# Kernel optimization log

Hardware: AMD Instinct MI355X
Metric: run time of the kernel (lower is better)

The kernel has to match this reference:

```python
import jax, jax.numpy as jnp
import numpy as np

D_MODEL = 1024
NUM_HEADS = 16
HEAD_DIM = D_MODEL // NUM_HEADS


def setup_inputs() -> dict:
    key = jax.random.key(0)
    k1, k2, k3, k4, k5 = jax.random.split(key, 5)
    B, S = 2, 2048
    X = jax.random.normal(k1, (B, S, D_MODEL), dtype=jnp.float32)
    Wqkv = jax.random.normal(k2, (3 * D_MODEL, D_MODEL), dtype=jnp.float32) * 0.02
    bqkv = jax.random.normal(k3, (3 * D_MODEL,), dtype=jnp.float32) * 0.02
    Wo = jax.random.normal(k4, (D_MODEL, D_MODEL), dtype=jnp.float32) * 0.02
    bo = jax.random.normal(k5, (D_MODEL,), dtype=jnp.float32) * 0.02
    return {"X": X, "Wqkv": Wqkv, "bqkv": bqkv, "Wo": Wo, "bo": bo}


def reference(X, Wqkv, bqkv, Wo, bo):
    B, S, D = X.shape
    # fused QKV projection (torch Linear: x @ W.T + b)
    qkv = X @ Wqkv.T + bqkv                                  # [B, S, 3D]
    qkv = qkv.reshape(B, S, NUM_HEADS, 3 * HEAD_DIM)
    qkv = jnp.transpose(qkv, (0, 2, 1, 3))                   # [B, H, S, 3*hd]
    q, k, v = jnp.split(qkv, 3, axis=-1)                     # each [B, H, S, hd]
    # naive scaled dot-product attention (materializes full SxS scores)
    scale = 1.0 / jnp.sqrt(jnp.asarray(HEAD_DIM, dtype=X.dtype))
    scores = jnp.einsum("bhqd,bhkd->bhqk", q, k) * scale     # [B, H, S, S]
    attn = jax.nn.softmax(scores, axis=-1)
    values = jnp.einsum("bhqk,bhkd->bhqd", attn, v)          # [B, H, S, hd]
    values = jnp.transpose(values, (0, 2, 1, 3)).reshape(B, S, D)
    return values @ Wo.T + bo
```

## Files before the change

kernel.cpp:

```cpp
#include <hip/hip_runtime.h>

#define DM    1024
#define NH    16
#define HD    64
#define SEQ   2048
#define BATCH 2
#define NQKV  3072
#define MTOT  4096

using half4 = __attribute__((ext_vector_type(4))) _Float16;
using half8 = __attribute__((ext_vector_type(8))) _Float16;
using f32x4 = __attribute__((ext_vector_type(4))) float;

typedef const __attribute__((address_space(1))) unsigned int* gp_t;
typedef __attribute__((address_space(3))) unsigned int* lp_t;

__device__ __forceinline__ void gl2lds16(const void* g, void* l) {
    __builtin_amdgcn_global_load_lds((gp_t)g, (lp_t)l, 16, 0, 0);
}

__device__ __forceinline__ f32x4 fzero4() {
    f32x4 v; v[0] = 0.f; v[1] = 0.f; v[2] = 0.f; v[3] = 0.f; return v;
}

__device__ __forceinline__ int sw8(int row, int col) {
    return (row << 6) | ((((col >> 3) ^ row) & 7) << 3) | (col & 7);
}
__device__ __forceinline__ int sw16(int row, int col) {
    return (row << 7) | ((((col >> 3) ^ row) & 15) << 3) | (col & 7);
}

__global__ __launch_bounds__(256) void cvt_f32_f16(const float* __restrict__ in,
                                                   _Float16* __restrict__ out, int n4) {
    int i = blockIdx.x * 256 + threadIdx.x;
    if (i >= n4) return;
    float4 f = reinterpret_cast<const float4*>(in)[i];
    half4 h;
    h[0] = (_Float16)f.x; h[1] = (_Float16)f.y;
    h[2] = (_Float16)f.z; h[3] = (_Float16)f.w;
    reinterpret_cast<half4*>(out)[i] = h;
}

template <bool OUT_F16>
__global__ __launch_bounds__(256) void gemm_nt(const _Float16* __restrict__ A,
                                               const _Float16* __restrict__ B,
                                               const float* __restrict__ bias,
                                               void* __restrict__ Cout,
                                               int M, int N, int K) {
    __shared__ _Float16 lA[128 * 64];
    __shared__ _Float16 lB[128 * 64];
    const int tid = threadIdx.x;
    const int m0 = blockIdx.y * 128, n0 = blockIdx.x * 128;
    const int wave = tid >> 6, lane = tid & 63, quad = lane >> 4, l15 = lane & 15;
    const int wm = (wave & 1) * 64, wn = (wave >> 1) * 64;

    f32x4 acc[4][4];
#pragma unroll
    for (int i = 0; i < 4; ++i)
#pragma unroll
        for (int j = 0; j < 4; ++j) acc[i][j] = fzero4();

    const int cperm = (((tid & 7) ^ (tid >> 3)) & 7) * 8;
    const _Float16* Ab = A + (long)(m0 + (tid >> 3)) * K + cperm;
    const _Float16* Bb = B + (long)(n0 + (tid >> 3)) * K + cperm;
    char* lAp = (char*)lA + tid * 16;
    char* lBp = (char*)lB + tid * 16;

    for (int kt = 0; kt < K; kt += 64) {
        __syncthreads();
#pragma unroll
        for (int j = 0; j < 4; ++j) {
            gl2lds16(Ab + (long)j * 32 * K + kt, lAp + j * 4096);
            gl2lds16(Bb + (long)j * 32 * K + kt, lBp + j * 4096);
        }
        __syncthreads();
#pragma unroll
        for (int ks = 0; ks < 2; ++ks) {
            half8 af[4], bfr[4];
#pragma unroll
            for (int t = 0; t < 4; ++t) {
                af[t]  = *(const half8*)(lA + sw8(wm + t * 16 + l15, ks * 32 + quad * 8));
                bfr[t] = *(const half8*)(lB + sw8(wn + t * 16 + l15, ks * 32 + quad * 8));
            }
#pragma unroll
            for (int mt = 0; mt < 4; ++mt)
#pragma unroll
                for (int nt = 0; nt < 4; ++nt)
                    acc[mt][nt] = __builtin_amdgcn_mfma_f32_16x16x32_f16(
                        af[mt], bfr[nt], acc[mt][nt], 0, 0, 0);
        }
    }

    float bs[4];
#pragma unroll
    for (int nt = 0; nt < 4; ++nt) bs[nt] = bias[n0 + wn + nt * 16 + l15];

#pragma unroll
    for (int mt = 0; mt < 4; ++mt) {
#pragma unroll
        for (int r = 0; r < 4; ++r) {
            const int m = m0 + wm + mt * 16 + quad * 4 + r;
#pragma unroll
            for (int nt = 0; nt < 4; ++nt) {
                const int n = n0 + wn + nt * 16 + l15;
                const float v = acc[mt][nt][r] + bs[nt];
                if constexpr (OUT_F16)
                    ((_Float16*)Cout)[(long)m * N + n] = (_Float16)v;
                else
                    ((float*)Cout)[(long)m * N + n] = v;
            }
        }
    }
}

__global__ __launch_bounds__(256) void repack_v(const _Float16* __restrict__ qkvh,
                                                _Float16* __restrict__ vt) {
    const int b = blockIdx.z, h = blockIdx.y, s0 = blockIdx.x * 32;
    const int d = threadIdx.x & 63, si = threadIdx.x >> 6;
    const _Float16* src = qkvh + (long)(b * SEQ + s0 + si * 8) * NQKV + h * 192 + 128 + d;
    half8 v;
#pragma unroll
    for (int i = 0; i < 8; ++i) v[i] = src[(long)i * NQKV];
    *(half8*)(vt + (long)((b * NH + h) * HD + d) * SEQ + s0 + si * 8) = v;
}

__global__ __launch_bounds__(256) void attn_flash(const _Float16* __restrict__ qkv,
                                                  const _Float16* __restrict__ vt,
                                                  _Float16* __restrict__ aout) {
    __shared__ _Float16 lQ[128 * 64];
    __shared__ _Float16 lK[128 * 64];
    __shared__ _Float16 lV[64 * 128];
    const int b = blockIdx.z, h = blockIdx.y, q0 = blockIdx.x * 128;
    const int tid = threadIdx.x;
    const int wave = tid >> 6, lane = tid & 63, quad = lane >> 4, l15 = lane & 15;
    const float CS = 0.18033688011112042f;

    const int cperm8  = (((tid & 7) ^ (tid >> 3)) & 7) * 8;
    const int cperm16 = (((tid & 15) ^ (tid >> 4)) & 15) * 8;

    const _Float16* qsrc = qkv + (long)(b * SEQ + q0 + (tid >> 3)) * NQKV + h * 192 + cperm8;
#pragma unroll
    for (int j = 0; j < 4; ++j)
        gl2lds16(qsrc + (long)j * 32 * NQKV, (char*)lQ + j * 4096 + tid * 16);
    __syncthreads();

    half8 qf[2][2];
#pragma unroll
    for (int qt = 0; qt < 2; ++qt)
#pragma unroll
        for (int ks = 0; ks < 2; ++ks)
            qf[qt][ks] = *(const half8*)(lQ + sw8(wave * 32 + qt * 16 + l15, ks * 32 + quad * 8));

    f32x4 O[2][4];
#pragma unroll
    for (int qt = 0; qt < 2; ++qt)
#pragma unroll
        for (int dt = 0; dt < 4; ++dt) O[qt][dt] = fzero4();
    float mst[2] = {-1e30f, -1e30f};
    float lst[2] = {0.f, 0.f};

    const _Float16* ksrc = qkv + (long)(b * SEQ + (tid >> 3)) * NQKV + h * 192 + 64 + cperm8;
    const _Float16* vsrc = vt + (long)((b * NH + h) * HD + (tid >> 4)) * SEQ + cperm16;

    for (int it = 0; it < 16; ++it) {
        const int s0 = it * 128;
        __syncthreads();
#pragma unroll
        for (int j = 0; j < 4; ++j) {
            gl2lds16(ksrc + (long)(s0 + j * 32) * NQKV, (char*)lK + j * 4096 + tid * 16);
            gl2lds16(vsrc + (long)j * 16 * SEQ + s0,    (char*)lV + j * 4096 + tid * 16);
        }
        __syncthreads();

        f32x4 st[2][8];
#pragma unroll
        for (int qt = 0; qt < 2; ++qt)
#pragma unroll
            for (int kt = 0; kt < 8; ++kt) st[qt][kt] = fzero4();
#pragma unroll
        for (int kt = 0; kt < 8; ++kt) {
#pragma unroll
            for (int ks = 0; ks < 2; ++ks) {
                half8 kf = *(const half8*)(lK + sw8(kt * 16 + l15, ks * 32 + quad * 8));
                st[0][kt] = __builtin_amdgcn_mfma_f32_16x16x32_f16(kf, qf[0][ks], st[0][kt], 0, 0, 0);
                st[1][kt] = __builtin_amdgcn_mfma_f32_16x16x32_f16(kf, qf[1][ks], st[1][kt], 0, 0, 0);
            }
        }

        float alpha[2];
#pragma unroll
        for (int qt = 0; qt < 2; ++qt) {
            float mc = -1e30f;
#pragma unroll
            for (int kt = 0; kt < 8; ++kt) {
                f32x4 s = st[qt][kt];
                mc = fmaxf(mc, fmaxf(fmaxf(s[0], s[1]), fmaxf(s[2], s[3])));
            }
            mc = fmaxf(mc, __shfl_xor(mc, 16));
            mc = fmaxf(mc, __shfl_xor(mc, 32));
            mc *= CS;
            const float mn = fmaxf(mst[qt], mc);
            alpha[qt] = __builtin_amdgcn_exp2f(mst[qt] - mn);
            mst[qt] = mn;
            float rs = 0.f;
#pragma unroll
            for (int kt = 0; kt < 8; ++kt) {
#pragma unroll
                for (int r = 0; r < 4; ++r) {
                    const float p = __builtin_amdgcn_exp2f(st[qt][kt][r] * CS - mn);
                    st[qt][kt][r] = p;
                    rs += p;
                }
            }
            rs += __shfl_xor(rs, 16);
            rs += __shfl_xor(rs, 32);
            lst[qt] = lst[qt] * alpha[qt] + rs;
        }

#pragma unroll
        for (int qt = 0; qt < 2; ++qt) {
#pragma unroll
            for (int r = 0; r < 4; ++r) {
                const float ar = __shfl(alpha[qt], quad * 4 + r);
#pragma unroll
                for (int dt = 0; dt < 4; ++dt) O[qt][dt][r] *= ar;
            }
        }

#pragma unroll
        for (int t = 0; t < 4; ++t) {
            half8 pf0, pf1;
#pragma unroll
            for (int r = 0; r < 4; ++r) {
                pf0[r]     = (_Float16)st[0][2 * t][r];
                pf0[4 + r] = (_Float16)st[0][2 * t + 1][r];
                pf1[r]     = (_Float16)st[1][2 * t][r];
                pf1[4 + r] = (_Float16)st[1][2 * t + 1][r];
            }
#pragma unroll
            for (int dt = 0; dt < 4; ++dt) {
                const int vrow = dt * 16 + l15;
                half4 v0 = *(const half4*)(lV + sw16(vrow, t * 32 + quad * 4));
                half4 v1 = *(const half4*)(lV + sw16(vrow, t * 32 + quad * 4 + 16));
                half8 vf = __builtin_shufflevector(v0, v1, 0, 1, 2, 3, 4, 5, 6, 7);
                O[0][dt] = __builtin_amdgcn_mfma_f32_16x16x32_f16(pf0, vf, O[0][dt], 0, 0, 0);
                O[1][dt] = __builtin_amdgcn_mfma_f32_16x16x32_f16(pf1, vf, O[1][dt], 0, 0, 0);
            }
        }
    }

#pragma unroll
    for (int qt = 0; qt < 2; ++qt) {
        const float linv = 1.0f / lst[qt];
#pragma unroll
        for (int r = 0; r < 4; ++r) {
            const float lr = __shfl(linv, quad * 4 + r);
            const int row = b * SEQ + q0 + wave * 32 + qt * 16 + quad * 4 + r;
#pragma unroll
            for (int dt = 0; dt < 4; ++dt)
                aout[(long)row * DM + h * HD + dt * 16 + l15] =
                    (_Float16)(O[qt][dt][r] * lr);
        }
    }
}

extern "C" void kernel_launch(void* const* d_in, const int* in_sizes, int n_in,
                              void* d_out, int out_size, void* d_ws, size_t ws_size,
                              hipStream_t stream) {
    const float* X    = (const float*)d_in[0];
    const float* Wqkv = (const float*)d_in[1];
    const float* bqkv = (const float*)d_in[2];
    const float* Wo   = (const float*)d_in[3];
    const float* bo   = (const float*)d_in[4];

    char* ws = (char*)d_ws;
    _Float16* Xh   = (_Float16*)(ws);
    _Float16* Wqh  = (_Float16*)(ws + (size_t)8  * 1048576);
    _Float16* Woh  = (_Float16*)(ws + (size_t)14 * 1048576);
    _Float16* qkvh = (_Float16*)(ws + (size_t)16 * 1048576);
    _Float16* vth  = (_Float16*)(ws + (size_t)40 * 1048576);
    _Float16* atth = (_Float16*)(ws + (size_t)48 * 1048576);

    cvt_f32_f16<<<(MTOT * DM / 4 + 255) / 256, 256, 0, stream>>>(X, Xh, MTOT * DM / 4);
    cvt_f32_f16<<<(NQKV * DM / 4 + 255) / 256, 256, 0, stream>>>(Wqkv, Wqh, NQKV * DM / 4);
    cvt_f32_f16<<<(DM * DM / 4 + 255) / 256, 256, 0, stream>>>(Wo, Woh, DM * DM / 4);

    gemm_nt<true><<<dim3(NQKV / 128, MTOT / 128), 256, 0, stream>>>(
        Xh, Wqh, bqkv, qkvh, MTOT, NQKV, DM);

    repack_v<<<dim3(SEQ / 32, NH, BATCH), 256, 0, stream>>>(qkvh, vth);

    attn_flash<<<dim3(SEQ / 128, NH, BATCH), 256, 0, stream>>>(qkvh, vth, atth);

    gemm_nt<false><<<dim3(DM / 128, MTOT / 128), 256, 0, stream>>>(
        atth, Woh, bo, d_out, MTOT, DM, DM);
}
```

Baseline: 207.3 us.

## Double-buffer attention K/V, compute row sums via MFMA, merge conversions, smaller output GEMM tile

The attention kernel now double-buffers its K/V tiles in shared memory. It prefetches the next block while computing on the current one, and reuses the K buffer to stage Q. Exponentials are computed with fused FMA and packed straight to fp16. Row sums come from an MFMA against a ones vector instead of scalar adds and shuffles, which also drops the final reciprocal shuffle. The three fp32-to-fp16 conversion launches are merged into one kernel writing a contiguous workspace, and the output projection uses a 64-row tile GEMM to double its block count. Together these aim to cut load stalls, VALU work in the softmax, launch overhead and under-filled output GEMM waves, at the cost of doubled attention LDS and slightly different rounding of the denominator.

```diff
diff --git a/kernel.cpp b/kernel.cpp
--- a/kernel.cpp
+++ b/kernel.cpp
@@ -8,9 +8,10 @@
 #define NQKV  3072
 #define MTOT  4096
 
-using half4 = __attribute__((ext_vector_type(4))) _Float16;
-using half8 = __attribute__((ext_vector_type(8))) _Float16;
-using f32x4 = __attribute__((ext_vector_type(4))) float;
+using half2v = __attribute__((ext_vector_type(2))) _Float16;
+using half4  = __attribute__((ext_vector_type(4))) _Float16;
+using half8  = __attribute__((ext_vector_type(8))) _Float16;
+using f32x4  = __attribute__((ext_vector_type(4))) float;
 
 typedef const __attribute__((address_space(1))) unsigned int* gp_t;
 typedef __attribute__((address_space(3))) unsigned int* lp_t;
@@ -30,11 +31,27 @@
     return (row << 7) | ((((col >> 3) ^ row) & 15) << 3) | (col & 7);
 }
 
-__global__ __launch_bounds__(256) void cvt_f32_f16(const float* __restrict__ in,
-                                                   _Float16* __restrict__ out, int n4) {
+#define CSCALE 0.18033688011112042f
+
+__device__ __forceinline__ half2v expk2(float a, float b, float negmn) {
+    return __builtin_bit_cast(half2v, __builtin_amdgcn_cvt_pkrtz(
+        __builtin_amdgcn_exp2f(__builtin_fmaf(a, CSCALE, negmn)),
+        __builtin_amdgcn_exp2f(__builtin_fmaf(b, CSCALE, negmn))));
+}
+
+__global__ __launch_bounds__(256) void cvt_all(const float* __restrict__ X,
+                                               const float* __restrict__ W1,
+                                               const float* __restrict__ W2,
+                                               _Float16* __restrict__ out) {
+    const int nX = MTOT * DM / 4, nW1 = NQKV * DM / 4, nW2 = DM * DM / 4;
     int i = blockIdx.x * 256 + threadIdx.x;
-    if (i >= n4) return;
-    float4 f = reinterpret_cast<const float4*>(in)[i];
+    if (i >= nX + nW1 + nW2) return;
+    const float* src;
+    int off;
+    if (i < nX)            { src = X;  off = i; }
+    else if (i < nX + nW1) { src = W1; off = i - nX; }
+    else                   { src = W2; off = i - nX - nW1; }
+    float4 f = reinterpret_cast<const float4*>(src)[off];
     half4 h;
     h[0] = (_Float16)f.x; h[1] = (_Float16)f.y;
     h[2] = (_Float16)f.z; h[3] = (_Float16)f.w;
@@ -113,6 +130,80 @@
     }
 }
 
+template <bool OUT_F16>
+__global__ __launch_bounds__(256) void gemm_nt_64(const _Float16* __restrict__ A,
+                                                  const _Float16* __restrict__ B,
+                                                  const float* __restrict__ bias,
+                                                  void* __restrict__ Cout,
+                                                  int M, int N, int K) {
+    __shared__ _Float16 lA[64 * 64];
+    __shared__ _Float16 lB[128 * 64];
+    const int tid = threadIdx.x;
+    const int m0 = blockIdx.y * 64, n0 = blockIdx.x * 128;
+    const int wave = tid >> 6, lane = tid & 63, quad = lane >> 4, l15 = lane & 15;
+    const int wm = (wave & 1) * 32, wn = (wave >> 1) * 64;
+
+    f32x4 acc[2][4];
+#pragma unroll
+    for (int i = 0; i < 2; ++i)
+#pragma unroll
+        for (int j = 0; j < 4; ++j) acc[i][j] = fzero4();
+
+    const int cperm = (((tid & 7) ^ (tid >> 3)) & 7) * 8;
+    const _Float16* Ab = A + (long)(m0 + (tid >> 3)) * K + cperm;
+    const _Float16* Bb = B + (long)(n0 + (tid >> 3)) * K + cperm;
+    char* lAp = (char*)lA + tid * 16;
+    char* lBp = (char*)lB + tid * 16;
+
+    for (int kt = 0; kt < K; kt += 64) {
+        __syncthreads();
+#pragma unroll
+        for (int j = 0; j < 2; ++j)
+            gl2lds16(Ab + (long)j * 32 * K + kt, lAp + j * 4096);
+#pragma unroll
+        for (int j = 0; j < 4; ++j)
+            gl2lds16(Bb + (long)j * 32 * K + kt, lBp + j * 4096);
+        __syncthreads();
+#pragma unroll
+        for (int ks = 0; ks < 2; ++ks) {
+            half8 af[2], bfr[4];
+#pragma unroll
+            for (int t = 0; t < 2; ++t)
+                af[t] = *(const half8*)(lA + sw8(wm + t * 16 + l15, ks * 32 + quad * 8));
+#pragma unroll
+            for (int t = 0; t < 4; ++t)
+                bfr[t] = *(const half8*)(lB + sw8(wn + t * 16 + l15, ks * 32 + quad * 8));
+#pragma unroll
+            for (int mt = 0; mt < 2; ++mt)
+#pragma unroll
+                for (int nt = 0; nt < 4; ++nt)
+                    acc[mt][nt] = __builtin_amdgcn_mfma_f32_16x16x32_f16(
+                        af[mt], bfr[nt], acc[mt][nt], 0, 0, 0);
+        }
+    }
+
+    float bs[4];
+#pragma unroll
+    for (int nt = 0; nt < 4; ++nt) bs[nt] = bias[n0 + wn + nt * 16 + l15];
+
+#pragma unroll
+    for (int mt = 0; mt < 2; ++mt) {
+#pragma unroll
+        for (int r = 0; r < 4; ++r) {
+            const int m = m0 + wm + mt * 16 + quad * 4 + r;
+#pragma unroll
+            for (int nt = 0; nt < 4; ++nt) {
+                const int n = n0 + wn + nt * 16 + l15;
+                const float v = acc[mt][nt][r] + bs[nt];
+                if constexpr (OUT_F16)
+                    ((_Float16*)Cout)[(long)m * N + n] = (_Float16)v;
+                else
+                    ((float*)Cout)[(long)m * N + n] = v;
+            }
+        }
+    }
+}
+
 __global__ __launch_bounds__(256) void repack_v(const _Float16* __restrict__ qkvh,
                                                 _Float16* __restrict__ vt) {
     const int b = blockIdx.z, h = blockIdx.y, s0 = blockIdx.x * 32;
@@ -127,13 +218,11 @@
 __global__ __launch_bounds__(256) void attn_flash(const _Float16* __restrict__ qkv,
                                                   const _Float16* __restrict__ vt,
                                                   _Float16* __restrict__ aout) {
-    __shared__ _Float16 lQ[128 * 64];
-    __shared__ _Float16 lK[128 * 64];
-    __shared__ _Float16 lV[64 * 128];
+    __shared__ _Float16 lK[2][128 * 64];
+    __shared__ _Float16 lV[2][64 * 128];
     const int b = blockIdx.z, h = blockIdx.y, q0 = blockIdx.x * 128;
     const int tid = threadIdx.x;
     const int wave = tid >> 6, lane = tid & 63, quad = lane >> 4, l15 = lane & 15;
-    const float CS = 0.18033688011112042f;
 
     const int cperm8  = (((tid & 7) ^ (tid >> 3)) & 7) * 8;
     const int cperm16 = (((tid & 15) ^ (tid >> 4)) & 15) * 8;
@@ -141,7 +230,7 @@
     const _Float16* qsrc = qkv + (long)(b * SEQ + q0 + (tid >> 3)) * NQKV + h * 192 + cperm8;
 #pragma unroll
     for (int j = 0; j < 4; ++j)
-        gl2lds16(qsrc + (long)j * 32 * NQKV, (char*)lQ + j * 4096 + tid * 16);
+        gl2lds16(qsrc + (long)j * 32 * NQKV, (char*)lK[0] + j * 4096 + tid * 16);
     __syncthreads();
 
     half8 qf[2][2];
@@ -149,28 +238,41 @@
     for (int qt = 0; qt < 2; ++qt)
 #pragma unroll
         for (int ks = 0; ks < 2; ++ks)
-            qf[qt][ks] = *(const half8*)(lQ + sw8(wave * 32 + qt * 16 + l15, ks * 32 + quad * 8));
+            qf[qt][ks] = *(const half8*)(lK[0] + sw8(wave * 32 + qt * 16 + l15, ks * 32 + quad * 8));
+    __syncthreads();
 
     f32x4 O[2][4];
 #pragma unroll
     for (int qt = 0; qt < 2; ++qt)
 #pragma unroll
         for (int dt = 0; dt < 4; ++dt) O[qt][dt] = fzero4();
+    f32x4 lsum[2] = {fzero4(), fzero4()};
     float mst[2] = {-1e30f, -1e30f};
-    float lst[2] = {0.f, 0.f};
+
+    half8 ones;
+#pragma unroll
+    for (int i = 0; i < 8; ++i) ones[i] = (_Float16)1.0f;
 
     const _Float16* ksrc = qkv + (long)(b * SEQ + (tid >> 3)) * NQKV + h * 192 + 64 + cperm8;
     const _Float16* vsrc = vt + (long)((b * NH + h) * HD + (tid >> 4)) * SEQ + cperm16;
 
+#pragma unroll
+    for (int j = 0; j < 4; ++j) {
+        gl2lds16(ksrc + (long)(j * 32) * NQKV, (char*)lK[0] + j * 4096 + tid * 16);
+        gl2lds16(vsrc + (long)j * 16 * SEQ,    (char*)lV[0] + j * 4096 + tid * 16);
+    }
+
+    int cur = 0;
     for (int it = 0; it < 16; ++it) {
-        const int s0 = it * 128;
-        __syncthreads();
-#pragma unroll
-        for (int j = 0; j < 4; ++j) {
-            gl2lds16(ksrc + (long)(s0 + j * 32) * NQKV, (char*)lK + j * 4096 + tid * 16);
-            gl2lds16(vsrc + (long)j * 16 * SEQ + s0,    (char*)lV + j * 4096 + tid * 16);
-        }
-        __syncthreads();
+        __syncthreads();
+        if (it < 15) {
+            const int s0n = (it + 1) * 128;
+#pragma unroll
+            for (int j = 0; j < 4; ++j) {
+                gl2lds16(ksrc + (long)(s0n + j * 32) * NQKV, (char*)lK[cur ^ 1] + j * 4096 + tid * 16);
+                gl2lds16(vsrc + (long)j * 16 * SEQ + s0n,    (char*)lV[cur ^ 1] + j * 4096 + tid * 16);
+            }
+        }
 
         f32x4 st[2][8];
 #pragma unroll
@@ -181,13 +283,13 @@
         for (int kt = 0; kt < 8; ++kt) {
 #pragma unroll
             for (int ks = 0; ks < 2; ++ks) {
-                half8 kf = *(const half8*)(lK + sw8(kt * 16 + l15, ks * 32 + quad * 8));
+                half8 kf = *(const half8*)(lK[cur] + sw8(kt * 16 + l15, ks * 32 + quad * 8));
                 st[0][kt] = __builtin_amdgcn_mfma_f32_16x16x32_f16(kf, qf[0][ks], st[0][kt], 0, 0, 0);
                 st[1][kt] = __builtin_amdgcn_mfma_f32_16x16x32_f16(kf, qf[1][ks], st[1][kt], 0, 0, 0);
             }
         }
 
-        float alpha[2];
+        float alpha[2], negmn[2];
 #pragma unroll
         for (int qt = 0; qt < 2; ++qt) {
             float mc = -1e30f;
@@ -198,23 +300,11 @@
             }
             mc = fmaxf(mc, __shfl_xor(mc, 16));
             mc = fmaxf(mc, __shfl_xor(mc, 32));
-            mc *= CS;
+            mc *= CSCALE;
             const float mn = fmaxf(mst[qt], mc);
             alpha[qt] = __builtin_amdgcn_exp2f(mst[qt] - mn);
             mst[qt] = mn;
-            float rs = 0.f;
-#pragma unroll
-            for (int kt = 0; kt < 8; ++kt) {
-#pragma unroll
-                for (int r = 0; r < 4; ++r) {
-                    const float p = __builtin_amdgcn_exp2f(st[qt][kt][r] * CS - mn);
-                    st[qt][kt][r] = p;
-                    rs += p;
-                }
-            }
-            rs += __shfl_xor(rs, 16);
-            rs += __shfl_xor(rs, 32);
-            lst[qt] = lst[qt] * alpha[qt] + rs;
+            negmn[qt] = -mn;
         }
 
 #pragma unroll
@@ -224,37 +314,42 @@
                 const float ar = __shfl(alpha[qt], quad * 4 + r);
 #pragma unroll
                 for (int dt = 0; dt < 4; ++dt) O[qt][dt][r] *= ar;
+                lsum[qt][r] *= ar;
             }
         }
 
 #pragma unroll
         for (int t = 0; t < 4; ++t) {
-            half8 pf0, pf1;
-#pragma unroll
-            for (int r = 0; r < 4; ++r) {
-                pf0[r]     = (_Float16)st[0][2 * t][r];
-                pf0[4 + r] = (_Float16)st[0][2 * t + 1][r];
-                pf1[r]     = (_Float16)st[1][2 * t][r];
-                pf1[4 + r] = (_Float16)st[1][2 * t + 1][r];
+            half8 pf[2];
+#pragma unroll
+            for (int qt = 0; qt < 2; ++qt) {
+                half2v p01 = expk2(st[qt][2 * t][0],     st[qt][2 * t][1],     negmn[qt]);
+                half2v p23 = expk2(st[qt][2 * t][2],     st[qt][2 * t][3],     negmn[qt]);
+                half2v p45 = expk2(st[qt][2 * t + 1][0], st[qt][2 * t + 1][1], negmn[qt]);
+                half2v p67 = expk2(st[qt][2 * t + 1][2], st[qt][2 * t + 1][3], negmn[qt]);
+                half4 lo = __builtin_shufflevector(p01, p23, 0, 1, 2, 3);
+                half4 hi = __builtin_shufflevector(p45, p67, 0, 1, 2, 3);
+                pf[qt] = __builtin_shufflevector(lo, hi, 0, 1, 2, 3, 4, 5, 6, 7);
+                lsum[qt] = __builtin_amdgcn_mfma_f32_16x16x32_f16(pf[qt], ones, lsum[qt], 0, 0, 0);
             }
 #pragma unroll
             for (int dt = 0; dt < 4; ++dt) {
                 const int vrow = dt * 16 + l15;
-                half4 v0 = *(const half4*)(lV + sw16(vrow, t * 32 + quad * 4));
-                half4 v1 = *(const half4*)(lV + sw16(vrow, t * 32 + quad * 4 + 16));
+                half4 v0 = *(const half4*)(lV[cur] + sw16(vrow, t * 32 + quad * 4));
+                half4 v1 = *(const half4*)(lV[cur] + sw16(vrow, t * 32 + quad * 4 + 16));
                 half8 vf = __builtin_shufflevector(v0, v1, 0, 1, 2, 3, 4, 5, 6, 7);
-                O[0][dt] = __builtin_amdgcn_mfma_f32_16x16x32_f16(pf0, vf, O[0][dt], 0, 0, 0);
-                O[1][dt] = __builtin_amdgcn_mfma_f32_16x16x32_f16(pf1, vf, O[1][dt], 0, 0, 0);
-            }
-        }
+                O[0][dt] = __builtin_amdgcn_mfma_f32_16x16x32_f16(pf[0], vf, O[0][dt], 0, 0, 0);
+                O[1][dt] = __builtin_amdgcn_mfma_f32_16x16x32_f16(pf[1], vf, O[1][dt], 0, 0, 0);
+            }
+        }
+        cur ^= 1;
     }
 
 #pragma unroll
     for (int qt = 0; qt < 2; ++qt) {
-        const float linv = 1.0f / lst[qt];
 #pragma unroll
         for (int r = 0; r < 4; ++r) {
-            const float lr = __shfl(linv, quad * 4 + r);
+            const float lr = 1.0f / lsum[qt][r];
             const int row = b * SEQ + q0 + wave * 32 + qt * 16 + quad * 4 + r;
 #pragma unroll
             for (int dt = 0; dt < 4; ++dt)
@@ -281,9 +376,8 @@
     _Float16* vth  = (_Float16*)(ws + (size_t)40 * 1048576);
     _Float16* atth = (_Float16*)(ws + (size_t)48 * 1048576);
 
-    cvt_f32_f16<<<(MTOT * DM / 4 + 255) / 256, 256, 0, stream>>>(X, Xh, MTOT * DM / 4);
-    cvt_f32_f16<<<(NQKV * DM / 4 + 255) / 256, 256, 0, stream>>>(Wqkv, Wqh, NQKV * DM / 4);
-    cvt_f32_f16<<<(DM * DM / 4 + 255) / 256, 256, 0, stream>>>(Wo, Woh, DM * DM / 4);
+    const int ncvt = (MTOT * DM + NQKV * DM + DM * DM) / 4;
+    cvt_all<<<(ncvt + 255) / 256, 256, 0, stream>>>(X, Wqkv, Wo, Xh);
 
     gemm_nt<true><<<dim3(NQKV / 128, MTOT / 128), 256, 0, stream>>>(
         Xh, Wqh, bqkv, qkvh, MTOT, NQKV, DM);
@@ -292,6 +386,6 @@
 
     attn_flash<<<dim3(SEQ / 128, NH, BATCH), 256, 0, stream>>>(qkvh, vth, atth);
 
-    gemm_nt<false><<<dim3(DM / 128, MTOT / 128), 256, 0, stream>>>(
+    gemm_nt_64<false><<<dim3(DM / 128, MTOT / 64), 256, 0, stream>>>(
         atth, Woh, bo, d_out, MTOT, DM, DM);
 }
```

Result: slower. 235.8 us (+13.8%).
